# Optimization experiments

Measured on AMD Instinct MI355X. Metric: run time of the kernel, lower is better.

The kernel has to match this reference:

```python
import jax, jax.numpy as jnp
import numpy as np

B = 100000
D = 32          # per-modality feature dim
SCALE = 1.0 / jnp.sqrt(2.0 * D)  # 1/sqrt(64)


def setup_inputs() -> dict:
    key = jax.random.key(0)
    k1, k2, k3, k4 = jax.random.split(key, 4)
    return {
        "f1_norm": jax.random.normal(k1, (B, D), dtype=jnp.float32),
        "f2_norm": jax.random.normal(k2, (B, D), dtype=jnp.float32),
        "W_ca": jax.random.normal(k3, (1, 2 * D), dtype=jnp.float32) * 0.1,
        "W_cv": jax.random.normal(k4, (1, 2 * D), dtype=jnp.float32) * 0.1,
    }


def reference(f1_norm, f2_norm, W_ca, W_cv):
    # av: concat of audio and visual feats, [B, 64]
    av = jnp.concatenate([f1_norm, f2_norm], axis=-1)
    # per-sample outer-product attention: aud_fts^T @ aud_vis_fts -> [B, 32, 64]
    audio_att = jnp.tanh(f1_norm[:, :, None] * av[:, None, :] * SCALE)
    vis_att = jnp.tanh(f2_norm[:, :, None] * av[:, None, :] * SCALE)
    # Linear(64,1,no bias): contract last dim with weight row -> [B, 32]
    H_a = 0.1 * jax.nn.relu(jnp.einsum('bij,j->bi', audio_att, W_ca[0]) + f1_norm)
    H_v = 0.1 * jax.nn.relu(jnp.einsum('bij,j->bi', vis_att, W_cv[0]) + f2_norm)
    # concat H_a^T, H_v^T per sample -> [B, 1, 64]
    return jnp.concatenate([H_a, H_v], axis=-1)[:, None, :]
```

## Files before the change

### kernel.cpp

```cpp
#include <hip/hip_runtime.h>
#include <hip/hip_fp16.h>
#include <math.h>


__device__ __forceinline__ float wave_ror1_f32(float v) {
    return __int_as_float(__builtin_amdgcn_update_dpp(
        __float_as_int(v), __float_as_int(v), 0x13C, 0xF, 0xF, false));
}

__device__ __forceinline__ float tanh_lut(const float* __restrict__ tb,
                                          float xs32, float a) {
    float idxf = fmaf(xs32, a, 1024.5f);
    idxf = __builtin_amdgcn_fmed3f(idxf, 0.0f, 2047.0f);
    return tb[(int)idxf];
}

__device__ __forceinline__ float tanh_sig(float xc, float a) {
    const float s = __builtin_amdgcn_rcpf(1.0f + __builtin_amdgcn_exp2f(xc * a));
    return fmaf(-2.0f, s, 1.0f);
}

__global__ __launch_bounds__(256, 4) void cam_kernel(
    const float* __restrict__ f1,
    const float* __restrict__ f2,
    const float* __restrict__ Wca,
    const float* __restrict__ Wcv,
    float* __restrict__ out,
    int B)
{
    constexpr float C = 0.3606737602222409f;

    __shared__ __half2 s_Qh[32][64];
    __shared__ float s_tanh[2048];

    const int tid  = threadIdx.x;
    const int lane = tid & 63;

    for (int i = tid; i < 2048; i += 256)
        s_tanh[i] = tanhf((float)(i - 1024) * 0.00390625f);

    for (int idx = tid; idx < 32 * 64; idx += 256) {
        const int k   = idx >> 6;
        const int ln  = idx & 63;
        const int sel = ln >> 5;
        const int j   = (ln + k) & 63;
        const float wo = (sel ? Wcv : Wca)[j];
        const float wd = ((j < 32) ? Wca : Wcv)[ln];
        s_Qh[k][ln] = __floats2half2_rn(wo, wd);
    }
    __syncthreads();

    const int sel = lane >> 5;
    const float* __restrict__ fbase = sel ? f2 : f1;
    const float* __restrict__ tb = s_tanh;
    const __half2* __restrict__ Qp = &s_Qh[0][lane];
    const int col = lane & 31;

    const float w0  = (sel ? Wcv : Wca)[lane];
    const float w32 = (sel ? Wcv : Wca)[lane ^ 32];
    const int idx31 = ((lane + 31) & 63) << 2;
    const int idx32 = (lane ^ 32) << 2;

    const int gw     = (blockIdx.x * 256 + tid) >> 6;
    const int stride = (gridDim.x << 2) * 2;

    int b = gw * 2;
    if (b >= B) return;
    float xA = fbase[b * 32 + col];
    float xB = (b + 1 < B) ? fbase[(b + 1) * 32 + col] : 0.0f;

    while (b < B) {
        const int bn = b + stride;
        float xnA = 0.0f, xnB = 0.0f;
        if (bn < B) {
            xnA = fbase[bn * 32 + col];
            if (bn + 1 < B) xnB = fbase[(bn + 1) * 32 + col];
        }

        const float xs32A = xA * 32.0f;
        const float xcB   = xB * C;
        float aA = __int_as_float(
            __builtin_amdgcn_ds_bpermute(idx31, __float_as_int(xA)));
        float aB = __int_as_float(
            __builtin_amdgcn_ds_bpermute(idx31, __float_as_int(xB)));
        const float a32A = __int_as_float(
            __builtin_amdgcn_ds_bpermute(idx32, __float_as_int(xA)));
        const float a32B = __int_as_float(
            __builtin_amdgcn_ds_bpermute(idx32, __float_as_int(xB)));

        float own0A = tanh_lut(tb, xs32A, xA)   * w0;
        float own0B = tanh_sig(xcB, xB)         * w0;
        float own1A = tanh_lut(tb, xs32A, a32A) * w32;
        float own1B = tanh_sig(xcB, a32B)       * w32;

        float tA = 0.0f, tB = 0.0f;
        #pragma unroll
        for (int k = 31; k >= 1; --k) {
            const float2 w2 = __half22float2(Qp[k * 64]);
            const float pA = tanh_lut(tb, xs32A, aA);
            const float pB = tanh_sig(xcB, aB);
            if (k & 1) { own0A = fmaf(pA, w2.x, own0A); own0B = fmaf(pB, w2.x, own0B); }
            else       { own1A = fmaf(pA, w2.x, own1A); own1B = fmaf(pB, w2.x, own1B); }
            tA = wave_ror1_f32(fmaf(pA, w2.y, tA));
            aA = wave_ror1_f32(aA);
            tB = wave_ror1_f32(fmaf(pB, w2.y, tB));
            aB = wave_ror1_f32(aB);
        }

        const float hA = fmaxf(xA + own0A + own1A + tA, 0.0f) * 0.1f;
        const float hB = fmaxf(xB + own0B + own1B + tB, 0.0f) * 0.1f;
        out[b * 64 + lane] = hA;
        if (b + 1 < B) out[(b + 1) * 64 + lane] = hB;

        b = bn;
        xA = xnA;
        xB = xnB;
    }
}

extern "C" void kernel_launch(void* const* d_in, const int* in_sizes, int n_in,
                              void* d_out, int out_size, void* d_ws, size_t ws_size,
                              hipStream_t stream) {
    const float* f1  = (const float*)d_in[0];
    const float* f2  = (const float*)d_in[1];
    const float* Wca = (const float*)d_in[2];
    const float* Wcv = (const float*)d_in[3];
    float* out = (float*)d_out;

    const int B = in_sizes[0] / 32;
    const int pairs = (B + 1) / 2;
    int blocks = (pairs + 3) / 4;
    if (blocks > 2048) blocks = 2048;
    if (blocks < 1) blocks = 1;

    cam_kernel<<<blocks, 256, 0, stream>>>(f1, f2, Wca, Wcv, out, B);
}
```

Before: 132.9 us.

## Replace shared-memory half2 weight table with DPP-rotated register weights, LUT tanh for both

The precomputed fp16 weight table in shared memory is removed. Per-step weights are now rebuilt in registers by rotating weight vectors and a mask with DPP alongside the activations. The second sample's tanh also switches from the exp/rcp sigmoid form to the shared-memory lookup table. This drops the table-building prologue and the per-step LDS weight loads, and uses fp32 weights instead of fp16. The cost is three extra DPP rotations per step and more LDS lookup traffic for the tanh table.

```diff
diff --git a/kernel.cpp b/kernel.cpp
--- a/kernel.cpp
+++ b/kernel.cpp
@@ -1,5 +1,4 @@
 #include <hip/hip_runtime.h>
-#include <hip/hip_fp16.h>
 #include <math.h>
 
 
@@ -15,11 +14,6 @@
     return tb[(int)idxf];
 }
 
-__device__ __forceinline__ float tanh_sig(float xc, float a) {
-    const float s = __builtin_amdgcn_rcpf(1.0f + __builtin_amdgcn_exp2f(xc * a));
-    return fmaf(-2.0f, s, 1.0f);
-}
-
 __global__ __launch_bounds__(256, 4) void cam_kernel(
     const float* __restrict__ f1,
     const float* __restrict__ f2,
@@ -28,9 +22,6 @@
     float* __restrict__ out,
     int B)
 {
-    constexpr float C = 0.3606737602222409f;
-
-    __shared__ __half2 s_Qh[32][64];
     __shared__ float s_tanh[2048];
 
     const int tid  = threadIdx.x;
@@ -38,28 +29,29 @@
 
     for (int i = tid; i < 2048; i += 256)
         s_tanh[i] = tanhf((float)(i - 1024) * 0.00390625f);
-
-    for (int idx = tid; idx < 32 * 64; idx += 256) {
-        const int k   = idx >> 6;
-        const int ln  = idx & 63;
-        const int sel = ln >> 5;
-        const int j   = (ln + k) & 63;
-        const float wo = (sel ? Wcv : Wca)[j];
-        const float wd = ((j < 32) ? Wca : Wcv)[ln];
-        s_Qh[k][ln] = __floats2half2_rn(wo, wd);
-    }
     __syncthreads();
 
     const int sel = lane >> 5;
     const float* __restrict__ fbase = sel ? f2 : f1;
     const float* __restrict__ tb = s_tanh;
-    const __half2* __restrict__ Qp = &s_Qh[0][lane];
     const int col = lane & 31;
 
-    const float w0  = (sel ? Wcv : Wca)[lane];
-    const float w32 = (sel ? Wcv : Wca)[lane ^ 32];
+    const float wcaR = Wca[lane];
+    const float wcvR = Wcv[lane];
+    const float dR   = wcaR - wcvR;
+    const float w0   = sel ? wcvR : wcaR;
+    const float w32  = (sel ? Wcv : Wca)[lane ^ 32];
+
     const int idx31 = ((lane + 31) & 63) << 2;
     const int idx32 = (lane ^ 32) << 2;
+
+    const float Va31 = __int_as_float(
+        __builtin_amdgcn_ds_bpermute(idx31, __float_as_int(wcaR)));
+    const float Vv31 = __int_as_float(
+        __builtin_amdgcn_ds_bpermute(idx31, __float_as_int(wcvR)));
+    const float M31 = __int_as_float(
+        __builtin_amdgcn_ds_bpermute(idx31,
+            __float_as_int((lane < 32) ? 1.0f : 0.0f)));
 
     const int gw     = (blockIdx.x * 256 + tid) >> 6;
     const int stride = (gridDim.x << 2) * 2;
@@ -78,7 +70,7 @@
         }
 
         const float xs32A = xA * 32.0f;
-        const float xcB   = xB * C;
+        const float xs32B = xB * 32.0f;
         float aA = __int_as_float(
             __builtin_amdgcn_ds_bpermute(idx31, __float_as_int(xA)));
         float aB = __int_as_float(
@@ -89,22 +81,27 @@
             __builtin_amdgcn_ds_bpermute(idx32, __float_as_int(xB)));
 
         float own0A = tanh_lut(tb, xs32A, xA)   * w0;
-        float own0B = tanh_sig(xcB, xB)         * w0;
+        float own0B = tanh_lut(tb, xs32B, xB)   * w0;
         float own1A = tanh_lut(tb, xs32A, a32A) * w32;
-        float own1B = tanh_sig(xcB, a32B)       * w32;
+        float own1B = tanh_lut(tb, xs32B, a32B) * w32;
 
+        float va = Va31, vv = Vv31, m = M31;
         float tA = 0.0f, tB = 0.0f;
         #pragma unroll
         for (int k = 31; k >= 1; --k) {
-            const float2 w2 = __half22float2(Qp[k * 64]);
+            const float wo = sel ? vv : va;
+            const float wd = fmaf(m, dR, wcvR);
             const float pA = tanh_lut(tb, xs32A, aA);
-            const float pB = tanh_sig(xcB, aB);
-            if (k & 1) { own0A = fmaf(pA, w2.x, own0A); own0B = fmaf(pB, w2.x, own0B); }
-            else       { own1A = fmaf(pA, w2.x, own1A); own1B = fmaf(pB, w2.x, own1B); }
-            tA = wave_ror1_f32(fmaf(pA, w2.y, tA));
+            const float pB = tanh_lut(tb, xs32B, aB);
+            if (k & 1) { own0A = fmaf(pA, wo, own0A); own0B = fmaf(pB, wo, own0B); }
+            else       { own1A = fmaf(pA, wo, own1A); own1B = fmaf(pB, wo, own1B); }
+            tA = wave_ror1_f32(fmaf(pA, wd, tA));
             aA = wave_ror1_f32(aA);
-            tB = wave_ror1_f32(fmaf(pB, w2.y, tB));
+            tB = wave_ror1_f32(fmaf(pB, wd, tB));
             aB = wave_ror1_f32(aB);
+            va = wave_ror1_f32(va);
+            vv = wave_ror1_f32(vv);
+            m  = wave_ror1_f32(m);
         }
 
         const float hA = fmaxf(xA + own0A + own1A + tA, 0.0f) * 0.1f;
```

After: 129.6 us. -2.5%, faster.
